# Kernel tuning notes

Measured on AMD Instinct MI355X. Metric: run time of the kernel, lower is better.

The kernel has to match this reference:

```python
import jax, jax.numpy as jnp
import numpy as np

B, N, D, H = 4, 512, 64, 8
DH = D // H  # head dim


def layernorm(x, g, b, eps=1e-5):
    m = x.mean(-1, keepdims=True)
    v = x.var(-1, keepdims=True)
    return (x - m) / jnp.sqrt(v + eps) * g + b


def setup_inputs() -> dict:
    key = jax.random.key(0)
    ks = jax.random.split(key, 24)
    s = 0.05
    inp = {
        "h": jax.random.normal(ks[0], (B, N, D), jnp.float32),
        "p": jax.random.normal(ks[1], (B, N, D), jnp.float32),
        "e": jax.random.normal(ks[2], (B, N, N, D), jnp.float32),
        "k_RW": jax.random.uniform(ks[3], (B, N, N), jnp.float32),
        "mask": jnp.ones((B, N), jnp.float32),
        "adj": jax.random.bernoulli(ks[4], 0.05, (B, N, N)),
        # attention projections (no bias)
        "W_Q": jax.random.normal(ks[5], (D, D), jnp.float32) * s,
        "W_K": jax.random.normal(ks[6], (D, D), jnp.float32) * s,
        "W_V": jax.random.normal(ks[7], (D, D), jnp.float32) * s,
        "W_Q2": jax.random.normal(ks[8], (D, D), jnp.float32) * s,
        "W_K2": jax.random.normal(ks[9], (D, D), jnp.float32) * s,
        "W_E": jax.random.normal(ks[10], (D, D), jnp.float32) * s,
        "W_E2": jax.random.normal(ks[11], (D, D), jnp.float32) * s,
        # output projection (bias=True in nn.Linear default)
        "O_W": jax.random.normal(ks[12], (D, D), jnp.float32) * s,
        "O_b": jnp.zeros((D,), jnp.float32),
        # layer norms
        "ln1_g": jnp.ones((D,), jnp.float32),
        "ln1_b": jnp.zeros((D,), jnp.float32),
        "ln2_g": jnp.ones((D,), jnp.float32),
        "ln2_b": jnp.zeros((D,), jnp.float32),
        # FFN
        "W_f1": jax.random.normal(ks[13], (D, 2 * D), jnp.float32) * s,
        "b_f1": jnp.zeros((2 * D,), jnp.float32),
        "W_f2": jax.random.normal(ks[14], (2 * D, D), jnp.float32) * s,
        "b_f2": jnp.zeros((D,), jnp.float32),
    }
    return inp


def reference(h, p, e, k_RW, mask, adj,
              W_Q, W_K, W_V, W_Q2, W_K2, W_E, W_E2,
              O_W, O_b, ln1_g, ln1_b, ln2_g, ln2_b,
              W_f1, b_f1, W_f2, b_f2):
    h_in1 = h
    # combine_h_p('sum') then layer_norm1
    x = layernorm(h + p, ln1_g, ln1_b)
    scale = DH ** -0.5

    def proj(W):  # [B,N,D] -> [B,N,H,DH]
        return (x @ W).reshape(B, N, H, DH)

    Q = proj(W_Q)
    K = proj(W_K) * scale
    Q2 = proj(W_Q2)
    K2 = proj(W_K2) * scale
    V = proj(W_V).transpose(0, 2, 1, 3)  # [B,H,N,DH]

    E = (e @ W_E).reshape(B, N, N, H, DH)
    E2 = (e @ W_E2).reshape(B, N, N, H, DH)
    ef = adj[:, :, :, None, None]  # edge_filter
    # double-attention: edge-gated three-way einsum on edges + complement
    scores = jnp.einsum('bihk,bjhk,bijhk->bhij', Q, K, jnp.where(ef, E, 0.0))
    scores = scores + jnp.einsum('bihk,bjhk,bijhk->bhij', Q2, K2,
                                 jnp.where(ef, 0.0, E2))

    # exp-softmax with global (per batch,head) max over both node dims
    scores = jnp.exp(scores - scores.max(axis=(-2, -1), keepdims=True))
    scores = scores * mask[:, None, :, None] * mask[:, None, None, :]
    scores = scores * k_RW[:, None, :, :]  # attention PE kernel
    denom = jnp.clip(scores.sum(-1, keepdims=True), 1e-6)

    att = (scores @ V) / denom  # [B,H,N,DH]
    h_att = att.transpose(0, 2, 1, 3).reshape(B, N, D)

    h2 = h_att @ O_W + O_b
    h2 = h_in1 + h2  # residual

    # feed_forward_block: pre-LN + FFN + residual
    y = layernorm(h2, ln2_g, ln2_b)
    y = jax.nn.relu(y @ W_f1 + b_f1) @ W_f2 + b_f2
    return h2 + y
```

## Files before the change

kernel.cpp:

```cpp
#include <hip/hip_runtime.h>
#include <stdint.h>


typedef __attribute__((ext_vector_type(8))) short short8;
typedef __attribute__((ext_vector_type(4))) float f32x4;

__device__ __forceinline__ unsigned short f2bf(float f) {
    unsigned int u = __float_as_uint(f);
    u = (u + 0x7fffu + ((u >> 16) & 1u)) >> 16;
    return (unsigned short)u;
}

__device__ __forceinline__ float wredsum(float v) {
    v += __shfl_xor(v, 1, 64);
    v += __shfl_xor(v, 2, 64);
    v += __shfl_xor(v, 4, 64);
    v += __shfl_xor(v, 8, 64);
    v += __shfl_xor(v, 16, 64);
    v += __shfl_xor(v, 32, 64);
    return v;
}

__global__ __launch_bounds__(256) void k1_ln_proj(
    const float* __restrict__ h, const float* __restrict__ p,
    const float* __restrict__ WQ, const float* __restrict__ WK,
    const float* __restrict__ WV, const float* __restrict__ WQ2,
    const float* __restrict__ WK2,
    const float* __restrict__ g1, const float* __restrict__ b1,
    float* __restrict__ Q1w, float* __restrict__ K1w,
    float* __restrict__ Vw, float* __restrict__ Q2w, float* __restrict__ K2w)
{
    __shared__ float xl[16][64];
    int tid = threadIdx.x, lane = tid & 63, w = tid >> 6;
    int row0 = blockIdx.x * 16;
    for (int rr = 0; rr < 4; ++rr) {
        int r = w * 4 + rr;
        int row = row0 + r;
        float v = h[row * 64 + lane] + p[row * 64 + lane];
        float m = wredsum(v) * (1.0f / 64.0f);
        float t = v - m;
        float var = wredsum(t * t) * (1.0f / 64.0f);
        xl[r][lane] = t * rsqrtf(var + 1e-5f) * g1[lane] + b1[lane];
    }
    __syncthreads();
    const float* Ws[5] = {WQ, WK, WV, WQ2, WK2};
    float* Os[5] = {Q1w, K1w, Vw, Q2w, K2w};
    const float scale = 0.35355339059327373f;
    for (int idx = tid; idx < 5 * 16 * 64; idx += 256) {
        int m = idx >> 10;
        int rem = idx & 1023;
        int r = rem >> 6;
        int c = rem & 63;
        const float* W = Ws[m];
        float acc = 0.f;
        #pragma unroll 8
        for (int d = 0; d < 64; ++d) acc += xl[r][d] * W[d * 64 + c];
        if (m == 1 || m == 4) acc *= scale;
        Os[m][(row0 + r) * 64 + c] = acc;
    }
}

__global__ __launch_bounds__(256) void k2_attn(
    const float* __restrict__ e, const int* __restrict__ adj,
    const float* __restrict__ kRW, const float* __restrict__ mask,
    const float* __restrict__ WE, const float* __restrict__ WE2,
    const float* __restrict__ Q1w, const float* __restrict__ K1w,
    const float* __restrict__ Q2w, const float* __restrict__ K2w,
    const float* __restrict__ Vw, float* __restrict__ hatt)
{
    __shared__ __align__(16) float EvL[4][16][132];
    __shared__ float red[4][4][18];
    int tid = threadIdx.x, lane = tid & 63, w = tid >> 6;
    int lm = lane & 15, lg = lane >> 4;
    int blk = blockIdx.x;
    int b = blk >> 9, i = blk & 511;
    const float mi = mask[b * 512 + i];

    short8 bf[2][4][2];
    {
        const float* Q1r = Q1w + (size_t)blk * 64;
        const float* Q2r = Q2w + (size_t)blk * 64;
        #pragma unroll
        for (int mat = 0; mat < 2; ++mat) {
            const float* W = mat ? WE2 : WE;
            const float* Qr = mat ? Q2r : Q1r;
            #pragma unroll
            for (int t = 0; t < 4; ++t) {
                int c = t * 16 + lm;
                float qv = Qr[c];
                #pragma unroll
                for (int s = 0; s < 2; ++s) {
                    short8 v;
                    #pragma unroll
                    for (int ei = 0; ei < 8; ++ei)
                        v[ei] = (short)f2bf(W[(s * 32 + lg * 8 + ei) * 64 + c] * qv);
                    bf[mat][t][s] = v;
                }
            }
        }
    }

    float nr[16];
    #pragma unroll
    for (int q = 0; q < 16; ++q) nr[q] = 0.f;
    float den0 = 0.f, den1 = 0.f;

    const float* eblk = e + (size_t)blk * 32768;
    int jl = lane >> 2, pp = lane & 3;

    for (int it = 0; it < 8; ++it) {
        int jbase = (it * 4 + w) * 16;
        const float* erow = eblk + (size_t)(jbase + lm) * 64 + lg * 8;
        float4 f0 = *(const float4*)(erow);
        float4 f1 = *(const float4*)(erow + 4);
        float4 f2v = *(const float4*)(erow + 32);
        float4 f3 = *(const float4*)(erow + 36);
        short8 a0, a1;
        a0[0]=(short)f2bf(f0.x); a0[1]=(short)f2bf(f0.y); a0[2]=(short)f2bf(f0.z); a0[3]=(short)f2bf(f0.w);
        a0[4]=(short)f2bf(f1.x); a0[5]=(short)f2bf(f1.y); a0[6]=(short)f2bf(f1.z); a0[7]=(short)f2bf(f1.w);
        a1[0]=(short)f2bf(f2v.x); a1[1]=(short)f2bf(f2v.y); a1[2]=(short)f2bf(f2v.z); a1[3]=(short)f2bf(f2v.w);
        a1[4]=(short)f2bf(f3.x); a1[5]=(short)f2bf(f3.y); a1[6]=(short)f2bf(f3.z); a1[7]=(short)f2bf(f3.w);

        #pragma unroll
        for (int mat = 0; mat < 2; ++mat) {
            #pragma unroll
            for (int t = 0; t < 4; ++t) {
                f32x4 acc = {0.f, 0.f, 0.f, 0.f};
                acc = __builtin_amdgcn_mfma_f32_16x16x32_bf16(a0, bf[mat][t][0], acc, 0, 0, 0);
                acc = __builtin_amdgcn_mfma_f32_16x16x32_bf16(a1, bf[mat][t][1], acc, 0, 0, 0);
                #pragma unroll
                for (int ei = 0; ei < 4; ++ei)
                    EvL[w][lg * 4 + ei][mat * 64 + t * 16 + lm] = acc[ei];
            }
        }
        __syncthreads();

        int j = jbase + jl;
        size_t pair = (size_t)blk * 512 + j;
        int av = adj[pair];
        float kk = kRW[pair];
        float mj = mask[b * 512 + j];
        size_t jrow = (size_t)(b * 512 + j) * 64 + pp * 16;
        const float* Ks = (av ? K1w : K2w) + jrow;
        const float* Vp = Vw + jrow;
        const float* Evp = &EvL[w][jl][(av ? 0 : 64) + pp * 16];

        float4 ev0 = *(const float4*)(Evp);
        float4 ev1 = *(const float4*)(Evp + 4);
        float4 ev2 = *(const float4*)(Evp + 8);
        float4 ev3 = *(const float4*)(Evp + 12);
        float4 ka = *(const float4*)(Ks);
        float4 kb = *(const float4*)(Ks + 4);
        float4 kc = *(const float4*)(Ks + 8);
        float4 kd = *(const float4*)(Ks + 12);
        float s0 = ev0.x*ka.x + ev0.y*ka.y + ev0.z*ka.z + ev0.w*ka.w
                 + ev1.x*kb.x + ev1.y*kb.y + ev1.z*kb.z + ev1.w*kb.w;
        float s1 = ev2.x*kc.x + ev2.y*kc.y + ev2.z*kc.z + ev2.w*kc.w
                 + ev3.x*kd.x + ev3.y*kd.y + ev3.z*kd.z + ev3.w*kd.w;
        float w0 = __expf(s0) * kk * mj * mi;
        float w1 = __expf(s1) * kk * mj * mi;

        float4 va = *(const float4*)(Vp);
        float4 vb = *(const float4*)(Vp + 4);
        float4 vc = *(const float4*)(Vp + 8);
        float4 vd = *(const float4*)(Vp + 12);
        nr[0] += w0 * va.x;  nr[1] += w0 * va.y;  nr[2] += w0 * va.z;  nr[3] += w0 * va.w;
        nr[4] += w0 * vb.x;  nr[5] += w0 * vb.y;  nr[6] += w0 * vb.z;  nr[7] += w0 * vb.w;
        nr[8] += w1 * vc.x;  nr[9] += w1 * vc.y;  nr[10] += w1 * vc.z; nr[11] += w1 * vc.w;
        nr[12] += w1 * vd.x; nr[13] += w1 * vd.y; nr[14] += w1 * vd.z; nr[15] += w1 * vd.w;
        den0 += w0; den1 += w1;
        __syncthreads();
    }

    #pragma unroll
    for (int q = 0; q < 16; ++q) {
        nr[q] += __shfl_xor(nr[q], 4, 64);
        nr[q] += __shfl_xor(nr[q], 8, 64);
        nr[q] += __shfl_xor(nr[q], 16, 64);
        nr[q] += __shfl_xor(nr[q], 32, 64);
    }
    den0 += __shfl_xor(den0, 4, 64); den0 += __shfl_xor(den0, 8, 64);
    den0 += __shfl_xor(den0, 16, 64); den0 += __shfl_xor(den0, 32, 64);
    den1 += __shfl_xor(den1, 4, 64); den1 += __shfl_xor(den1, 8, 64);
    den1 += __shfl_xor(den1, 16, 64); den1 += __shfl_xor(den1, 32, 64);

    if (jl == 0) {
        #pragma unroll
        for (int q = 0; q < 16; ++q) red[w][pp][q] = nr[q];
        red[w][pp][16] = den0;
        red[w][pp][17] = den1;
    }
    __syncthreads();
    if (tid < 64) {
        int p2 = tid >> 4, q = tid & 15;
        float ns = red[0][p2][q] + red[1][p2][q] + red[2][p2][q] + red[3][p2][q];
        int di = 16 + (q >> 3);
        float ds = red[0][p2][di] + red[1][p2][di] + red[2][p2][di] + red[3][p2][di];
        hatt[(size_t)blk * 64 + p2 * 16 + q] = ns / fmaxf(ds, 1e-6f);
    }
}

__global__ __launch_bounds__(256) void k3_out(
    const float* __restrict__ hatt, const float* __restrict__ h,
    const float* __restrict__ OW, const float* __restrict__ Ob,
    const float* __restrict__ g2, const float* __restrict__ b2,
    const float* __restrict__ Wf1, const float* __restrict__ bf1,
    const float* __restrict__ Wf2, const float* __restrict__ bf2,
    float* __restrict__ out)
{
    __shared__ float S[4][256];
    int tid = threadIdx.x, lane = tid & 63, w = tid >> 6;
    int row = blockIdx.x * 4 + w;
    S[w][lane] = hatt[(size_t)row * 64 + lane];
    __syncthreads();
    float h2 = h[(size_t)row * 64 + lane] + Ob[lane];
    #pragma unroll 8
    for (int k = 0; k < 64; ++k) h2 += S[w][k] * OW[k * 64 + lane];
    float m = wredsum(h2) * (1.f / 64.f);
    float t = h2 - m;
    float var = wredsum(t * t) * (1.f / 64.f);
    float y = t * rsqrtf(var + 1e-5f) * g2[lane] + b2[lane];
    S[w][64 + lane] = y;
    __syncthreads();
    float u1 = bf1[lane], u2 = bf1[64 + lane];
    #pragma unroll 8
    for (int k = 0; k < 64; ++k) {
        float yk = S[w][64 + k];
        u1 += yk * Wf1[k * 128 + lane];
        u2 += yk * Wf1[k * 128 + 64 + lane];
    }
    S[w][128 + lane] = fmaxf(u1, 0.f);
    S[w][192 + lane] = fmaxf(u2, 0.f);
    __syncthreads();
    float f = bf2[lane];
    #pragma unroll 8
    for (int c = 0; c < 128; ++c) f += S[w][128 + c] * Wf2[c * 64 + lane];
    out[(size_t)row * 64 + lane] = h2 + f;
}

extern "C" void kernel_launch(void* const* d_in, const int* in_sizes, int n_in,
                              void* d_out, int out_size, void* d_ws, size_t ws_size,
                              hipStream_t stream)
{
    const float* h   = (const float*)d_in[0];
    const float* p   = (const float*)d_in[1];
    const float* e   = (const float*)d_in[2];
    const float* kRW = (const float*)d_in[3];
    const float* mask= (const float*)d_in[4];
    const int*   adj = (const int*)d_in[5];
    const float* WQ  = (const float*)d_in[6];
    const float* WK  = (const float*)d_in[7];
    const float* WV  = (const float*)d_in[8];
    const float* WQ2 = (const float*)d_in[9];
    const float* WK2 = (const float*)d_in[10];
    const float* WE  = (const float*)d_in[11];
    const float* WE2 = (const float*)d_in[12];
    const float* OW  = (const float*)d_in[13];
    const float* Ob  = (const float*)d_in[14];
    const float* g1  = (const float*)d_in[15];
    const float* b1  = (const float*)d_in[16];
    const float* g2  = (const float*)d_in[17];
    const float* b2  = (const float*)d_in[18];
    const float* Wf1 = (const float*)d_in[19];
    const float* bf1 = (const float*)d_in[20];
    const float* Wf2 = (const float*)d_in[21];
    const float* bf2 = (const float*)d_in[22];
    float* out = (float*)d_out;

    float* ws = (float*)d_ws;
    float* Q1w = ws;
    float* K1w = ws + 131072;
    float* Q2w = ws + 262144;
    float* K2w = ws + 393216;
    float* Vw  = ws + 524288;
    float* hatt= ws + 655360;

    k1_ln_proj<<<128, 256, 0, stream>>>(h, p, WQ, WK, WV, WQ2, WK2, g1, b1,
                                        Q1w, K1w, Vw, Q2w, K2w);
    k2_attn<<<2048, 256, 0, stream>>>(e, adj, kRW, mask, WE, WE2,
                                      Q1w, K1w, Q2w, K2w, Vw, hatt);
    k3_out<<<512, 256, 0, stream>>>(hatt, h, OW, Ob, g2, b2, Wf1, bf1, Wf2, bf2, out);
}
```

Baseline: 511.0 us.

## Prefetch next edge tile in attention loop, drop barriers, shrink projection blocks

The attention kernel now software-pipelines its main loop. It loads the next iteration's edge rows plus the adj, kRW and mask values into registers while the current tile is converted and multiplied, and the loop is unrolled. Both per-iteration __syncthreads are removed, since each wave only reads back its own EvL slice in LDS. The first projection kernel now processes 8 rows per block over 256 blocks instead of 16 rows over 128, to raise parallelism. The prefetch raises register pressure, and dropping the barriers relies on each wave's LDS accesses staying in program order.

```diff
diff --git a/kernel.cpp b/kernel.cpp
--- a/kernel.cpp
+++ b/kernel.cpp
@@ -30,11 +30,11 @@
     float* __restrict__ Q1w, float* __restrict__ K1w,
     float* __restrict__ Vw, float* __restrict__ Q2w, float* __restrict__ K2w)
 {
-    __shared__ float xl[16][64];
+    __shared__ float xl[8][64];
     int tid = threadIdx.x, lane = tid & 63, w = tid >> 6;
-    int row0 = blockIdx.x * 16;
-    for (int rr = 0; rr < 4; ++rr) {
-        int r = w * 4 + rr;
+    int row0 = blockIdx.x * 8;
+    for (int rr = 0; rr < 2; ++rr) {
+        int r = w * 2 + rr;
         int row = row0 + r;
         float v = h[row * 64 + lane] + p[row * 64 + lane];
         float m = wredsum(v) * (1.0f / 64.0f);
@@ -46,9 +46,9 @@
     const float* Ws[5] = {WQ, WK, WV, WQ2, WK2};
     float* Os[5] = {Q1w, K1w, Vw, Q2w, K2w};
     const float scale = 0.35355339059327373f;
-    for (int idx = tid; idx < 5 * 16 * 64; idx += 256) {
-        int m = idx >> 10;
-        int rem = idx & 1023;
+    for (int idx = tid; idx < 5 * 8 * 64; idx += 256) {
+        int m = idx >> 9;
+        int rem = idx & 511;
         int r = rem >> 6;
         int c = rem & 63;
         const float* W = Ws[m];
@@ -73,8 +73,8 @@
     int tid = threadIdx.x, lane = tid & 63, w = tid >> 6;
     int lm = lane & 15, lg = lane >> 4;
     int blk = blockIdx.x;
-    int b = blk >> 9, i = blk & 511;
-    const float mi = mask[b * 512 + i];
+    int b = blk >> 9;
+    const float mi = mask[(size_t)blk];
 
     short8 bf[2][4][2];
     {
@@ -108,13 +108,41 @@
     const float* eblk = e + (size_t)blk * 32768;
     int jl = lane >> 2, pp = lane & 3;
 
+    float4 pf0, pf1, pf2, pf3;
+    int pav; float pkk, pmj;
+    {
+        int jbase = w * 16;
+        const float* erow = eblk + (size_t)(jbase + lm) * 64 + lg * 8;
+        pf0 = *(const float4*)(erow);
+        pf1 = *(const float4*)(erow + 4);
+        pf2 = *(const float4*)(erow + 32);
+        pf3 = *(const float4*)(erow + 36);
+        int j = jbase + jl;
+        size_t pair = (size_t)blk * 512 + j;
+        pav = adj[pair];
+        pkk = kRW[pair];
+        pmj = mask[b * 512 + j];
+    }
+
+    #pragma unroll
     for (int it = 0; it < 8; ++it) {
+        float4 f0 = pf0, f1 = pf1, f2v = pf2, f3 = pf3;
+        int av = pav; float kk = pkk, mj = pmj;
+        if (it < 7) {
+            int jb2 = ((it + 1) * 4 + w) * 16;
+            const float* erow = eblk + (size_t)(jb2 + lm) * 64 + lg * 8;
+            pf0 = *(const float4*)(erow);
+            pf1 = *(const float4*)(erow + 4);
+            pf2 = *(const float4*)(erow + 32);
+            pf3 = *(const float4*)(erow + 36);
+            int j2 = jb2 + jl;
+            size_t pair2 = (size_t)blk * 512 + j2;
+            pav = adj[pair2];
+            pkk = kRW[pair2];
+            pmj = mask[b * 512 + j2];
+        }
         int jbase = (it * 4 + w) * 16;
-        const float* erow = eblk + (size_t)(jbase + lm) * 64 + lg * 8;
-        float4 f0 = *(const float4*)(erow);
-        float4 f1 = *(const float4*)(erow + 4);
-        float4 f2v = *(const float4*)(erow + 32);
-        float4 f3 = *(const float4*)(erow + 36);
+
         short8 a0, a1;
         a0[0]=(short)f2bf(f0.x); a0[1]=(short)f2bf(f0.y); a0[2]=(short)f2bf(f0.z); a0[3]=(short)f2bf(f0.w);
         a0[4]=(short)f2bf(f1.x); a0[5]=(short)f2bf(f1.y); a0[6]=(short)f2bf(f1.z); a0[7]=(short)f2bf(f1.w);
@@ -133,13 +161,9 @@
                     EvL[w][lg * 4 + ei][mat * 64 + t * 16 + lm] = acc[ei];
             }
         }
-        __syncthreads();
 
         int j = jbase + jl;
-        size_t pair = (size_t)blk * 512 + j;
-        int av = adj[pair];
-        float kk = kRW[pair];
-        float mj = mask[b * 512 + j];
+        float mj_i = mj * mi;
         size_t jrow = (size_t)(b * 512 + j) * 64 + pp * 16;
         const float* Ks = (av ? K1w : K2w) + jrow;
         const float* Vp = Vw + jrow;
@@ -157,8 +181,8 @@
                  + ev1.x*kb.x + ev1.y*kb.y + ev1.z*kb.z + ev1.w*kb.w;
         float s1 = ev2.x*kc.x + ev2.y*kc.y + ev2.z*kc.z + ev2.w*kc.w
                  + ev3.x*kd.x + ev3.y*kd.y + ev3.z*kd.z + ev3.w*kd.w;
-        float w0 = __expf(s0) * kk * mj * mi;
-        float w1 = __expf(s1) * kk * mj * mi;
+        float w0 = __expf(s0) * kk * mj_i;
+        float w1 = __expf(s1) * kk * mj_i;
 
         float4 va = *(const float4*)(Vp);
         float4 vb = *(const float4*)(Vp + 4);
@@ -169,7 +193,6 @@
         nr[8] += w1 * vc.x;  nr[9] += w1 * vc.y;  nr[10] += w1 * vc.z; nr[11] += w1 * vc.w;
         nr[12] += w1 * vd.x; nr[13] += w1 * vd.y; nr[14] += w1 * vd.z; nr[15] += w1 * vd.w;
         den0 += w0; den1 += w1;
-        __syncthreads();
     }
 
     #pragma unroll
@@ -275,7 +298,7 @@
     float* Vw  = ws + 524288;
     float* hatt= ws + 655360;
 
-    k1_ln_proj<<<128, 256, 0, stream>>>(h, p, WQ, WK, WV, WQ2, WK2, g1, b1,
+    k1_ln_proj<<<256, 256, 0, stream>>>(h, p, WQ, WK, WV, WQ2, WK2, g1, b1,
                                         Q1w, K1w, Vw, Q2w, K2w);
     k2_attn<<<2048, 256, 0, stream>>>(e, adj, kRW, mask, WE, WE2,
                                       Q1w, K1w, Q2w, K2w, Vw, hatt);
```

Result: faster. 479.4 us (-6.2%).
